# Optimization experiments

Hardware: AMD Instinct MI355X
Metric: run time of the kernel (lower is better)

The kernel has to match this reference:

```python
import jax, jax.numpy as jnp
import numpy as np

NUM_CLASS = 3
SCORE_THRESH = 0.1
NMS_THRESH = 0.25
PRE = 512    # NMS_PRE_MAXSIZE (reduced from 4096 for memory; same algorithm)
POST = 100   # NMS_POST_MAXSIZE
EPS = 1e-8


def _cross(a, b):
    return a[..., 0] * b[..., 1] - a[..., 1] * b[..., 0]


def _corners(box):
    # box: (7,) = (x, y, z, dx, dy, dz, heading) -> BEV corners (4,2), CCW
    x, y, dx, dy, r = box[0], box[1], box[3], box[4], box[6]
    c, s = jnp.cos(r), jnp.sin(r)
    lx = jnp.array([0.5, -0.5, -0.5, 0.5]) * dx
    ly = jnp.array([0.5, 0.5, -0.5, -0.5]) * dy
    return jnp.stack([x + lx * c - ly * s, y + lx * s + ly * c], axis=-1)


def _in_box(pts, box):
    # pts (P,2): point-in-rotated-rect test in the box frame
    px, py = pts[:, 0] - box[0], pts[:, 1] - box[1]
    c, s = jnp.cos(box[6]), jnp.sin(box[6])
    u = px * c + py * s
    v = -px * s + py * c
    return (jnp.abs(u) <= box[3] * 0.5 + 1e-5) & (jnp.abs(v) <= box[4] * 0.5 + 1e-5)


def _bev_inter_area(ba, bb):
    # Exact rotated-rect intersection area (same construction as the CUDA
    # iou3d kernel: inside corners + edge intersections, angle-sorted shoelace).
    ca, cb = _corners(ba), _corners(bb)
    pa, ra = ca, jnp.roll(ca, -1, 0) - ca       # edges of a
    pb, rb = cb, jnp.roll(cb, -1, 0) - cb       # edges of b
    d = _cross(ra[:, None, :], rb[None, :, :])  # (4,4)
    dsafe = jnp.where(jnp.abs(d) > EPS, d, 1.0)
    qp = pb[None, :, :] - pa[:, None, :]
    t = _cross(qp, rb[None, :, :]) / dsafe
    u = _cross(qp, ra[:, None, :]) / dsafe
    vi = (jnp.abs(d) > EPS) & (t >= 0.0) & (t <= 1.0) & (u >= 0.0) & (u <= 1.0)
    ip = pa[:, None, :] + t[..., None] * ra[:, None, :]  # (4,4,2)
    pts = jnp.concatenate([ca, cb, ip.reshape(16, 2)], 0)          # (24,2)
    val = jnp.concatenate([_in_box(ca, bb), _in_box(cb, ba), vi.reshape(16)], 0)
    cnt = val.sum()
    ctr = (pts * val[:, None]).sum(0) / jnp.maximum(cnt, 1)
    ang = jnp.where(val, jnp.arctan2(pts[:, 1] - ctr[1], pts[:, 0] - ctr[0]), 1e9)
    o = jnp.argsort(ang)
    ps, vs = pts[o], val[o]
    ps = jnp.where(vs[:, None], ps, ps[0])  # collapse invalid onto first valid pt
    area = 0.5 * jnp.abs(_cross(ps, jnp.roll(ps, -1, 0)).sum())
    return jnp.where(cnt >= 3, area, 0.0)


def _iou3d(ba, bb):
    inter = _bev_inter_area(ba, bb)
    zt = jnp.minimum(ba[2] + ba[5] * 0.5, bb[2] + bb[5] * 0.5)
    zb = jnp.maximum(ba[2] - ba[5] * 0.5, bb[2] - bb[5] * 0.5)
    i3 = inter * jnp.maximum(zt - zb, 0.0)
    va = ba[3] * ba[4] * ba[5]
    vb = bb[3] * bb[4] * bb[5]
    return i3 / jnp.maximum(va + vb - i3, EPS)


_iou_mat = jax.vmap(jax.vmap(_iou3d, (None, 0)), (0, None))


def _nms(scores, boxes):
    # scores (K,) sorted descending; greedy suppression in score order
    valid = scores >= SCORE_THRESH
    iou = _iou_mat(boxes, boxes)  # (K,K)

    def body(sup, inp):
        row, v, i = inp
        keep = v & jnp.logical_not(sup[i])
        sup = sup | (keep & (row > NMS_THRESH))
        return sup, keep

    K = scores.shape[0]
    _, keep = jax.lax.scan(body, jnp.zeros((K,), bool), (iou, valid, jnp.arange(K)))
    return keep


def _post_one(cls_logits, boxes):
    # multi_classes_nms path: cls_preds_normalized=False -> sigmoid
    scores = jax.nn.sigmoid(cls_logits)  # (N, NUM_CLASS)
    out_b, out_s, out_l = [], [], []
    for k in range(NUM_CLASS):
        s = jnp.where(scores[:, k] >= SCORE_THRESH, scores[:, k], -1.0)
        top_s, idx = jax.lax.top_k(s, PRE)
        b = boxes[idx]
        keep = _nms(top_s, b)
        ks = jnp.where(keep, top_s, -1.0)
        os_, oi = jax.lax.top_k(ks, POST)
        ov = os_ >= SCORE_THRESH
        out_b.append(jnp.where(ov[:, None], b[oi], 0.0))
        out_s.append(jnp.where(ov, os_, 0.0))
        out_l.append((k + 1) * ov.astype(jnp.int32))  # final_labels = k + 1
    return (jnp.concatenate(out_b, 0), jnp.concatenate(out_s, 0),
            jnp.concatenate(out_l, 0))


def setup_inputs() -> dict:
    key = jax.random.key(0)
    k1, k2 = jax.random.split(key)
    B, N = 2, 100000
    batch_cls_preds = jax.random.normal(k1, (B, N, NUM_CLASS), dtype=jnp.float32)
    u = jax.random.uniform(k2, (B, N, 7), dtype=jnp.float32)
    x = u[..., 0] * 70.0
    y = u[..., 1] * 80.0 - 40.0
    z = u[..., 2] * 2.0 - 1.0
    dx = u[..., 3] * 3.0 + 1.5
    dy = u[..., 4] * 1.5 + 1.2
    dz = u[..., 5] * 1.0 + 1.3
    r = u[..., 6] * 2.0 * np.pi - np.pi
    batch_box_preds = jnp.stack([x, y, z, dx, dy, dz, r], axis=-1)
    return {"batch_cls_preds": batch_cls_preds, "batch_box_preds": batch_box_preds}


def reference(batch_cls_preds, batch_box_preds):
    # returns per-batch padded (pred_boxes (B, 3*POST, 7), pred_scores, pred_labels);
    # invalid slots are zeroed (label 0 == no detection)
    return jax.vmap(_post_one)(batch_cls_preds, batch_box_preds)
```

## Files before the change

### kernel.cpp

```cpp
#include <hip/hip_runtime.h>
#include <cstdint>

#define NCLS 3
#define NPTS 100000
#define NB 2
#define PRE 512
#define POST 100
#define SCORE_TH 0.1f
#define NMS_TH 0.25
#define CAP 1024
#define NBINS 384
#define BIN_SH 17
#define BIN_OFFW (0xBD000000u >> BIN_SH)
#define FMARG 2e-5f
#define NPROB (NB * NCLS)
#define NCHUNK 98
#define CPB 4
#define NKB 25
#define WAVES_PER_PROB 2304


__device__ __forceinline__ uint32_t score_key(float x)
{
    double sd = 1.0 / (1.0 + exp(-(double)x));
    float s = (float)sd;
    if (!(s >= SCORE_TH)) s = -1.0f;
    uint32_t u = __float_as_uint(s);
    return (u & 0x80000000u) ? ~u : (u | 0x80000000u);
}

__device__ __forceinline__ float fast_sig(float x)
{
    return 1.0f / (1.0f + __expf(-x));
}

__device__ __forceinline__ int fast_bin(float s)
{
    float v = (s >= SCORE_TH) ? s : -1.0f;
    uint32_t u = __float_as_uint(v);
    uint32_t kk = (u & 0x80000000u) ? ~u : (u | 0x80000000u);
    int b = (int)(kk >> BIN_SH) - (int)BIN_OFFW;
    return b < 0 ? 0 : (b > NBINS - 1 ? NBINS - 1 : b);
}

__global__ __launch_bounds__(1024) void hist_kernel(
    const float* __restrict__ cls, uint32_t* __restrict__ hist_part,
    uint32_t* __restrict__ ctrs)
{
    __shared__ uint32_t lh[NCLS][2][NBINS];
    const int tid = threadIdx.x;
    for (int t = tid; t < NCLS * 2 * NBINS; t += 1024) ((uint32_t*)lh)[t] = 0;
    if (blockIdx.x == 0 && tid < 8) ctrs[tid] = 0;
    __syncthreads();

    const int b = blockIdx.x / NKB, kb = blockIdx.x % NKB;
    const int par = (tid >> 6) & 1;
    const float* base = cls + (size_t)b * NPTS * NCLS;
    #pragma unroll
    for (int c = 0; c < CPB; ++c) {
        int i = (kb * CPB + c) * 1024 + tid;
        if (i < NPTS) {
            const float* cp = base + (size_t)i * NCLS;
            #pragma unroll
            for (int k = 0; k < NCLS; ++k)
                atomicAdd(&lh[k][par][fast_bin(fast_sig(cp[k]))], 1u);
        }
    }
    __syncthreads();
    uint32_t* P = hist_part + (size_t)((b * NKB + kb) * NCLS) * NBINS;
    for (int t = tid; t < NCLS * NBINS; t += 1024)
        P[t] = lh[t / NBINS][0][t % NBINS] + lh[t / NBINS][1][t % NBINS];
}

__global__ __launch_bounds__(1024) void compact_kernel(
    const float* __restrict__ cls, const uint32_t* __restrict__ hist_part,
    uint32_t* __restrict__ ctrs, unsigned long long* __restrict__ cand)
{
    const int p = blockIdx.x / NCHUNK, cb = blockIdx.x % NCHUNK;
    const int b = p / NCLS, k = p % NCLS;
    const int tid = threadIdx.x;

    __shared__ unsigned long long stage[1024];
    __shared__ uint32_t sbins[NBINS];
    __shared__ uint32_t lcnt, lbase, pivot_s;

    if (tid < NBINS) sbins[tid] = 0;
    if (tid == 0) { lcnt = 0; pivot_s = 0; }
    __syncthreads();

    for (int idx = tid; idx < NKB * NBINS; idx += 1024) {
        int kb = idx / NBINS, bin = idx % NBINS;
        uint32_t v = hist_part[(size_t)((b * NKB + kb) * NCLS + k) * NBINS + bin];
        if (v) atomicAdd(&sbins[bin], v);
    }
    __syncthreads();
    for (int off = 1; off < NBINS; off <<= 1) {
        uint32_t v = 0;
        if (tid < NBINS && tid + off < NBINS) v = sbins[tid + off];
        __syncthreads();
        if (tid < NBINS) sbins[tid] += v;
        __syncthreads();
    }
    if (tid < NBINS && sbins[tid] >= PRE &&
        (tid == NBINS - 1 || sbins[tid + 1] < PRE))
        pivot_s = (uint32_t)tid;
    __syncthreads();
    const uint32_t pb = pivot_s;

    const int i = cb * 1024 + tid;
    bool sv = false;
    unsigned long long entry = 0;
    if (i < NPTS) {
        float x = cls[((size_t)b * NPTS + i) * NCLS + k];
        float sfv = fast_sig(x);
        if ((uint32_t)fast_bin(sfv + FMARG) >= pb) {
            uint32_t kk = score_key(x);
            entry = ((unsigned long long)kk << 32) | (uint32_t)(~(uint32_t)i);
            sv = true;
        }
    }
    if (sv) { uint32_t s = atomicAdd(&lcnt, 1u); stage[s] = entry; }
    __syncthreads();
    if (tid == 0 && lcnt) lbase = atomicAdd(&ctrs[p], lcnt);
    __syncthreads();
    const uint32_t n = lcnt;
    if (n) {
        const uint32_t bs = lbase;
        for (uint32_t e = tid; e < n; e += 1024) {
            uint32_t g = bs + e;
            if (g < CAP) cand[(size_t)p * CAP + g] = stage[e];
        }
    }
}

__global__ __launch_bounds__(1024) void sort_geom_kernel(
    const float* __restrict__ boxes, const unsigned long long* __restrict__ cand,
    const uint32_t* __restrict__ ctrs, uint32_t* __restrict__ cand_idx,
    float* __restrict__ cand_score, double* __restrict__ boxdata,
    float* __restrict__ screen)
{
    const int p = blockIdx.x, b = p / NCLS;
    const int tid = threadIdx.x;
    __shared__ unsigned long long skey[CAP];

    const int cnt0 = (int)ctrs[p];
    const int cnt = cnt0 < CAP ? cnt0 : CAP;
    unsigned long long val = (tid < cnt) ? cand[(size_t)p * CAP + tid] : 0ull;
    __syncthreads();

    for (int k2 = 2; k2 <= CAP; k2 <<= 1) {
        const bool up = (tid & k2) == 0;
        for (int j = k2 >> 1; j >= 64; j >>= 1) {
            skey[tid] = val;
            __syncthreads();
            unsigned long long o = skey[tid ^ j];
            __syncthreads();
            const bool keepLarge = (((tid & j) == 0) == up);
            val = keepLarge ? (val >= o ? val : o) : (val <= o ? val : o);
        }
        int js = (k2 >> 1) < 32 ? (k2 >> 1) : 32;
        for (int j = js; j >= 1; j >>= 1) {
            unsigned long long o = __shfl_xor(val, j);
            const bool keepLarge = (((tid & j) == 0) == up);
            val = keepLarge ? (val >= o ? val : o) : (val <= o ? val : o);
        }
    }

    if (tid >= PRE) return;
    unsigned long long key = val;
    double* D = boxdata + (size_t)(p * PRE + tid) * 20;
    float* S = screen + (size_t)(p * PRE + tid) * 8;
    if (key == 0ull) {
        cand_idx[p * PRE + tid] = 0;
        cand_score[p * PRE + tid] = -1.0f;
        #pragma unroll
        for (int m = 0; m < 20; ++m) D[m] = 0.0;
        #pragma unroll
        for (int m = 0; m < 8; ++m) S[m] = 0.0f;
        return;
    }
    uint32_t idx = ~((uint32_t)key);
    uint32_t ov = (uint32_t)(key >> 32);
    uint32_t ub = (ov & 0x80000000u) ? (ov ^ 0x80000000u) : ~ov;
    float sc = __uint_as_float(ub);
    cand_idx[p * PRE + tid] = idx;
    cand_score[p * PRE + tid] = sc;

    const float* bp = boxes + ((size_t)b * NPTS + idx) * 7;
    double x = bp[0], y = bp[1], z = bp[2];
    double dx = bp[3], dy = bp[4], dz = bp[5], r = bp[6];
    double c = cos(r), s = sin(r);
    double hx = 0.5 * dx, hy = 0.5 * dy;
    double zlo = z - 0.5 * dz, zhi = z + 0.5 * dz;
    double rad = sqrt(hx * hx + hy * hy);
    D[0] = x; D[1] = y; D[2] = c; D[3] = s; D[4] = hx; D[5] = hy;
    D[6] = zlo; D[7] = zhi; D[8] = dx * dy * dz; D[9] = rad;
    const double lxs[4] = { hx, -hx, -hx,  hx };
    const double lys[4] = { hy,  hy, -hy, -hy };
    #pragma unroll
    for (int m = 0; m < 4; ++m) {
        D[10 + m] = x + lxs[m] * c - lys[m] * s;
        D[14 + m] = y + lxs[m] * s + lys[m] * c;
    }
    S[0] = (float)x; S[1] = (float)y; S[2] = (float)zlo; S[3] = (float)zhi;
    S[4] = (float)rad; S[5] = 0.0f; S[6] = 0.0f; S[7] = 0.0f;
}

__global__ __launch_bounds__(256) void iou_kernel(
    const float* __restrict__ screen, const double* __restrict__ boxdata,
    unsigned long long* __restrict__ mask)
{
    const int W = blockIdx.x * 4 + (threadIdx.x >> 6);
    const int lane = threadIdx.x & 63;
    const int prob = W / WAVES_PER_PROB;
    int t = W - prob * WAVES_PER_PROB;
    int cell = t >> 6, r = t & 63;
    int wi = 0;
    while (cell >= 8 - wi) { cell -= 8 - wi; ++wi; }
    const int wj = wi + cell;
    const int bi = wi * 64 + r;
    const int j = wj * 64 + lane;

    bool surv = false;
    {
        const float* SA = screen + (size_t)(prob * PRE + bi) * 8;
        const float* SB = screen + (size_t)(prob * PRE + j) * 8;
        if (j > bi) {
            float4 a4 = *(const float4*)SA;
            float4 b4 = *(const float4*)SB;
            float hz = fminf(a4.w, b4.w) - fmaxf(a4.z, b4.z);
            if (hz > 0.0f) {
                float ddx = a4.x - b4.x, ddy = a4.y - b4.y;
                float rs = SA[4] + SB[4] + 0.01f;
                surv = (ddx * ddx + ddy * ddy <= rs * rs);
            }
        }
    }
    unsigned long long sm = __ballot(surv);
    unsigned long long supw = 0ull;
    const double* A = boxdata + (size_t)(prob * PRE + bi) * 20;

    while (sm) {
        int jb = __ffsll(sm) - 1;
        sm &= sm - 1ull;
        const int bj = wj * 64 + jb;
        const double* B = boxdata + (size_t)(prob * PRE + bj) * 20;

        double hzd = fmin(A[7], B[7]) - fmax(A[6], B[6]);
        if (hzd <= 0.0) continue;
        {
            double ddx = B[0] - A[0], ddy = B[1] - A[1];
            double ca = A[2], sa = A[3], cb2 = B[2], sb2 = B[3];
            double cd = fabs(ca * cb2 + sa * sb2);
            double sd = fabs(sa * cb2 - ca * sb2);
            double pax = fabs(ddx * ca + ddy * sa);
            double pay = fabs(-ddx * sa + ddy * ca);
            double pbx = fabs(ddx * cb2 + ddy * sb2);
            double pby = fabs(-ddx * sb2 + ddy * cb2);
            if (pax > A[4] + B[4] * cd + B[5] * sd) continue;
            if (pay > A[5] + B[4] * sd + B[5] * cd) continue;
            if (pbx > B[4] + A[4] * cd + A[5] * sd) continue;
            if (pby > B[5] + A[4] * sd + A[5] * cd) continue;
            double areaA = 4.0 * A[4] * A[5], areaB = 4.0 * B[4] * B[5];
            double i3m = fmin(areaA, areaB) * hzd;
            double den = A[8] + B[8] - i3m;
            if (den < 1e-8) den = 1e-8;
            if (!(i3m / den > (double)NMS_TH)) continue;
        }

        double PX = 0.0, PY = 0.0;
        bool valid = false;
        if (lane < 8) {
            const double* S = (lane < 4) ? A : B;
            const double* O = (lane < 4) ? B : A;
            int m = lane & 3;
            PX = S[10 + m]; PY = S[14 + m];
            double rx = PX - O[0], ry = PY - O[1];
            double u =  rx * O[2] + ry * O[3];
            double v = -rx * O[3] + ry * O[2];
            valid = (fabs(u) <= O[4] + 1e-5) && (fabs(v) <= O[5] + 1e-5);
        } else if (lane < 24) {
            int e = lane - 8, m = e >> 2, nn = e & 3;
            double ax = A[10 + m], ay = A[14 + m];
            double rax = A[10 + ((m + 1) & 3)] - ax;
            double ray = A[14 + ((m + 1) & 3)] - ay;
            double bx = B[10 + nn], by = B[14 + nn];
            double rbx = B[10 + ((nn + 1) & 3)] - bx;
            double rby = B[14 + ((nn + 1) & 3)] - by;
            double d = rax * rby - ray * rbx;
            if (fabs(d) > 1e-8) {
                double qx = bx - ax, qy = by - ay;
                double tt = (qx * rby - qy * rbx) / d;
                double uu = (qx * ray - qy * rax) / d;
                valid = (tt >= 0.0 && tt <= 1.0 && uu >= 0.0 && uu <= 1.0);
                PX = ax + tt * rax; PY = ay + tt * ray;
            }
        }
        if (!valid) { PX = 0.0; PY = 0.0; }

        unsigned long long bal = __ballot(valid);
        int cnt = __popcll(bal);
        double sx = PX, sy = PY;
        #pragma unroll
        for (int off = 16; off; off >>= 1) {
            sx += __shfl_xor(sx, off);
            sy += __shfl_xor(sy, off);
        }
        int cdiv = cnt > 0 ? cnt : 1;
        double cxc = sx / cdiv, cyc = sy / cdiv;

        double ang = valid ? atan2(PY - cyc, PX - cxc) : 1e9;
        int sidx = lane;

        #pragma unroll
        for (int k = 2; k <= 32; k <<= 1) {
            #pragma unroll
            for (int jj = k >> 1; jj > 0; jj >>= 1) {
                double oang = __shfl_xor(ang, jj);
                double opx  = __shfl_xor(PX, jj);
                double opy  = __shfl_xor(PY, jj);
                int    oidx = __shfl_xor(sidx, jj);
                bool iLow = (lane & jj) == 0;
                bool dirUp = (lane & k) == 0;
                bool mineFirst = (ang < oang) || (ang == oang && sidx < oidx);
                bool keepMine = (mineFirst == (iLow == dirUp));
                if (!keepMine) { ang = oang; PX = opx; PY = opy; sidx = oidx; }
            }
        }

        double nxp = __shfl(PX, (lane + 1) & 31);
        double nyp = __shfl(PY, (lane + 1) & 31);
        double fx  = __shfl(PX, 0);
        double fy  = __shfl(PY, 0);
        bool last = (lane == cnt - 1);
        double qx = last ? fx : nxp, qy = last ? fy : nyp;
        double contrib = 0.0;
        if (lane < cnt)
            contrib = (PX - cxc) * (qy - cyc) - (PY - cyc) * (qx - cxc);
        #pragma unroll
        for (int off = 16; off; off >>= 1) contrib += __shfl_xor(contrib, off);
        double inter = (cnt >= 3) ? 0.5 * fabs(contrib) : 0.0;

        if (lane == 0) {
            double zt = fmin(A[7], B[7]);
            double zb = fmax(A[6], B[6]);
            double hz = zt - zb;
            bool sup = false;
            if (hz > 0.0) {
                double i3 = inter * hz;
                double den = A[8] + B[8] - i3;
                if (den < 1e-8) den = 1e-8;
                sup = (i3 / den) > (double)NMS_TH;
            }
            if (sup) supw |= 1ull << jb;
        }
    }

    if (lane == 0)
        mask[(size_t)(prob * PRE + bi) * 8 + wj] = supw;
}

__global__ __launch_bounds__(256) void nms_out_kernel(
    const float* __restrict__ boxes, const uint32_t* __restrict__ cand_idx,
    const float* __restrict__ cand_score,
    const unsigned long long* __restrict__ mask, float* __restrict__ out)
{
    const int p = blockIdx.x;
    const int b = p / NCLS, k = p % NCLS;
    const int tid = threadIdx.x;

    __shared__ unsigned long long smask[PRE * 8];
    __shared__ float sscore[PRE];
    __shared__ int slist[POST];
    __shared__ int scnt;

    for (int w = tid; w < PRE * 8; w += 256)
        smask[w] = mask[(size_t)p * PRE * 8 + w];
    for (int i = tid; i < PRE; i += 256)
        sscore[i] = cand_score[p * PRE + i];
    __syncthreads();

    if (tid < 64) {
        const int ln = tid;
        unsigned long long rem = 0ull;
        #pragma unroll
        for (int w = 0; w < 8; ++w) {
            unsigned long long bw = __ballot(sscore[w * 64 + ln] >= SCORE_TH);
            if (ln == w) rem = bw;
        }
        int c = 0;
        for (;;) {
            int cv = rem ? ((ln << 6) + (__ffsll(rem) - 1)) : 4096;
            int o1 = __shfl_xor(cv, 1); cv = cv < o1 ? cv : o1;
            int o2 = __shfl_xor(cv, 2); cv = cv < o2 ? cv : o2;
            int o4 = __shfl_xor(cv, 4); cv = cv < o4 ? cv : o4;
            int i = __shfl(cv, 0);
            if (i >= 4096) break;
            if (ln == 0) slist[c] = i;
            ++c;
            if (c >= POST) break;
            unsigned long long mm = (ln < 8) ? smask[i * 8 + ln] : 0ull;
            if (ln == (i >> 6)) mm |= 1ull << (i & 63);
            rem &= ~mm;
        }
        if (ln == 0) scnt = c;
    }
    __syncthreads();

    const int cnt2 = scnt;
    for (int t2 = tid; t2 < POST; t2 += 256) {
        int row = b * (NCLS * POST) + k * POST + t2;
        float* ob = out + (size_t)row * 7;
        float* os = out + (size_t)NB * NCLS * POST * 7 + row;
        float* ol = out + (size_t)NB * NCLS * POST * 7 + (size_t)NB * NCLS * POST + row;
        if (t2 < cnt2) {
            int rr = slist[t2];
            uint32_t idx = cand_idx[p * PRE + rr];
            const float* bp = boxes + ((size_t)b * NPTS + idx) * 7;
            #pragma unroll
            for (int c7 = 0; c7 < 7; ++c7) ob[c7] = bp[c7];
            *os = sscore[rr];
            *ol = (float)(k + 1);
        } else {
            #pragma unroll
            for (int c7 = 0; c7 < 7; ++c7) ob[c7] = 0.0f;
            *os = 0.0f;
            *ol = 0.0f;
        }
    }
}

extern "C" void kernel_launch(void* const* d_in, const int* in_sizes, int n_in,
                              void* d_out, int out_size, void* d_ws, size_t ws_size,
                              hipStream_t stream)
{
    (void)in_sizes; (void)n_in; (void)out_size; (void)ws_size;
    const float* cls   = (const float*)d_in[0];
    const float* boxes = (const float*)d_in[1];
    float* out = (float*)d_out;

    char* ws = (char*)d_ws;
    uint32_t* hist_part   = (uint32_t*)(ws);
    uint32_t* ctrs        = (uint32_t*)(ws + 230400);
    unsigned long long* cand = (unsigned long long*)(ws + 230528);
    unsigned long long* mask = (unsigned long long*)(ws + 279680);
    uint32_t* cand_idx    = (uint32_t*)(ws + 476288);
    float*    cand_score  = (float*)   (ws + 488576);
    double*   boxdata     = (double*)  (ws + 500864);
    float*    screen      = (float*)   (ws + 992384);

    hipLaunchKernelGGL(hist_kernel, dim3(NB * NKB), dim3(1024), 0, stream,
                       cls, hist_part, ctrs);
    hipLaunchKernelGGL(compact_kernel, dim3(NPROB * NCHUNK), dim3(1024),
                       0, stream, cls, hist_part, ctrs, cand);
    hipLaunchKernelGGL(sort_geom_kernel, dim3(NPROB), dim3(1024), 0, stream,
                       boxes, cand, ctrs, cand_idx, cand_score, boxdata, screen);
    hipLaunchKernelGGL(iou_kernel, dim3(NPROB * WAVES_PER_PROB / 4),
                       dim3(256), 0, stream, screen, boxdata, mask);
    hipLaunchKernelGGL(nms_out_kernel, dim3(NPROB), dim3(256), 0, stream,
                       boxes, cand_idx, cand_score, mask, out);
}
```

Before: 142.6 us.

## Fuse five-kernel NMS pipeline into one persistent block per class-batch problem

Replaces the histogram, compaction, sort, IoU and NMS kernels with a single kernel that runs one 1024-thread block per (batch, class) problem. The IoU mask, screen data and candidates now stay in shared memory, and the histogram bins raw logits instead of sigmoids, which is valid because sigmoid is monotonic. This removes launch overhead and global round-trips between stages. In exchange only 6 blocks run, so each block scans 100k scores twice serially and does all the pairwise IoU work on its own, leaving most of the GPU idle.

New measurement: 408.2 us. 2.86x slower.

```diff
diff --git a/kernel.cpp b/kernel.cpp
--- a/kernel.cpp
+++ b/kernel.cpp
@@ -10,13 +10,11 @@
 #define NMS_TH 0.25
 #define CAP 1024
 #define NBINS 384
-#define BIN_SH 17
-#define BIN_OFFW (0xBD000000u >> BIN_SH)
-#define FMARG 2e-5f
+#define XBIN_SH 16
+#define XBIN_OFF (0xBFC00000u >> XBIN_SH)
+#define XMARG 2e-3f
 #define NPROB (NB * NCLS)
 #define NCHUNK 98
-#define CPB 4
-#define NKB 25
 #define WAVES_PER_PROB 2304
 
 
@@ -29,71 +27,50 @@
     return (u & 0x80000000u) ? ~u : (u | 0x80000000u);
 }
 
-__device__ __forceinline__ float fast_sig(float x)
+__device__ __forceinline__ int xbin(float x)
 {
-    return 1.0f / (1.0f + __expf(-x));
-}
-
-__device__ __forceinline__ int fast_bin(float s)
-{
-    float v = (s >= SCORE_TH) ? s : -1.0f;
-    uint32_t u = __float_as_uint(v);
-    uint32_t kk = (u & 0x80000000u) ? ~u : (u | 0x80000000u);
-    int b = (int)(kk >> BIN_SH) - (int)BIN_OFFW;
+    uint32_t u = __float_as_uint(x);
+    uint32_t key = (u & 0x80000000u) ? ~u : (u | 0x80000000u);
+    int b = (int)(key >> XBIN_SH) - (int)XBIN_OFF;
     return b < 0 ? 0 : (b > NBINS - 1 ? NBINS - 1 : b);
 }
 
-__global__ __launch_bounds__(1024) void hist_kernel(
-    const float* __restrict__ cls, uint32_t* __restrict__ hist_part,
-    uint32_t* __restrict__ ctrs)
+__global__ __launch_bounds__(1024) void mega_kernel(
+    const float* __restrict__ cls, const float* __restrict__ boxes,
+    double* __restrict__ boxdata, float* __restrict__ out)
 {
-    __shared__ uint32_t lh[NCLS][2][NBINS];
-    const int tid = threadIdx.x;
-    for (int t = tid; t < NCLS * 2 * NBINS; t += 1024) ((uint32_t*)lh)[t] = 0;
-    if (blockIdx.x == 0 && tid < 8) ctrs[tid] = 0;
-    __syncthreads();
-
-    const int b = blockIdx.x / NKB, kb = blockIdx.x % NKB;
-    const int par = (tid >> 6) & 1;
-    const float* base = cls + (size_t)b * NPTS * NCLS;
-    #pragma unroll
-    for (int c = 0; c < CPB; ++c) {
-        int i = (kb * CPB + c) * 1024 + tid;
-        if (i < NPTS) {
-            const float* cp = base + (size_t)i * NCLS;
-            #pragma unroll
-            for (int k = 0; k < NCLS; ++k)
-                atomicAdd(&lh[k][par][fast_bin(fast_sig(cp[k]))], 1u);
-        }
-    }
-    __syncthreads();
-    uint32_t* P = hist_part + (size_t)((b * NKB + kb) * NCLS) * NBINS;
-    for (int t = tid; t < NCLS * NBINS; t += 1024)
-        P[t] = lh[t / NBINS][0][t % NBINS] + lh[t / NBINS][1][t % NBINS];
-}
-
-__global__ __launch_bounds__(1024) void compact_kernel(
-    const float* __restrict__ cls, const uint32_t* __restrict__ hist_part,
-    uint32_t* __restrict__ ctrs, unsigned long long* __restrict__ cand)
-{
-    const int p = blockIdx.x / NCHUNK, cb = blockIdx.x % NCHUNK;
+    const int p = blockIdx.x;
     const int b = p / NCLS, k = p % NCLS;
     const int tid = threadIdx.x;
-
-    __shared__ unsigned long long stage[1024];
+    const int lane = tid & 63;
+    const int wv = tid >> 6;
+
+    __shared__ unsigned long long skey[CAP];
+    __shared__ unsigned long long smask[PRE * 8];
     __shared__ uint32_t sbins[NBINS];
-    __shared__ uint32_t lcnt, lbase, pivot_s;
-
-    if (tid < NBINS) sbins[tid] = 0;
+    __shared__ float sx_l[PRE], sy_l[PRE];
+    __shared__ float szlo[PRE], szhi[PRE], srad[PRE];
+    __shared__ float sscore[PRE];
+    __shared__ uint32_t sidx[PRE];
+    __shared__ int slist[POST];
+    __shared__ int scnt;
+    __shared__ uint32_t lcnt, pivot_s;
+
+    const float* cp = cls + ((size_t)b * NPTS) * NCLS + k;
+    double* Dbase = boxdata + (size_t)p * PRE * 20;
+
+    for (int t = tid; t < NBINS; t += 1024) sbins[t] = 0;
     if (tid == 0) { lcnt = 0; pivot_s = 0; }
     __syncthreads();
-
-    for (int idx = tid; idx < NKB * NBINS; idx += 1024) {
-        int kb = idx / NBINS, bin = idx % NBINS;
-        uint32_t v = hist_part[(size_t)((b * NKB + kb) * NCLS + k) * NBINS + bin];
-        if (v) atomicAdd(&sbins[bin], v);
-    }
-    __syncthreads();
+    for (int ch = 0; ch < NCHUNK; ++ch) {
+        int i = ch * 1024 + tid;
+        if (i < NPTS) {
+            int bn = xbin(cp[(size_t)i * NCLS]);
+            if (bn > 0) atomicAdd(&sbins[bn], 1u);
+        }
+    }
+    __syncthreads();
+
     for (int off = 1; off < NBINS; off <<= 1) {
         uint32_t v = 0;
         if (tid < NBINS && tid + off < NBINS) v = sbins[tid + off];
@@ -105,48 +82,26 @@
         (tid == NBINS - 1 || sbins[tid + 1] < PRE))
         pivot_s = (uint32_t)tid;
     __syncthreads();
-    const uint32_t pb = pivot_s;
-
-    const int i = cb * 1024 + tid;
-    bool sv = false;
-    unsigned long long entry = 0;
-    if (i < NPTS) {
-        float x = cls[((size_t)b * NPTS + i) * NCLS + k];
-        float sfv = fast_sig(x);
-        if ((uint32_t)fast_bin(sfv + FMARG) >= pb) {
-            uint32_t kk = score_key(x);
-            entry = ((unsigned long long)kk << 32) | (uint32_t)(~(uint32_t)i);
-            sv = true;
-        }
-    }
-    if (sv) { uint32_t s = atomicAdd(&lcnt, 1u); stage[s] = entry; }
-    __syncthreads();
-    if (tid == 0 && lcnt) lbase = atomicAdd(&ctrs[p], lcnt);
-    __syncthreads();
-    const uint32_t n = lcnt;
-    if (n) {
-        const uint32_t bs = lbase;
-        for (uint32_t e = tid; e < n; e += 1024) {
-            uint32_t g = bs + e;
-            if (g < CAP) cand[(size_t)p * CAP + g] = stage[e];
-        }
-    }
-}
-
-__global__ __launch_bounds__(1024) void sort_geom_kernel(
-    const float* __restrict__ boxes, const unsigned long long* __restrict__ cand,
-    const uint32_t* __restrict__ ctrs, uint32_t* __restrict__ cand_idx,
-    float* __restrict__ cand_score, double* __restrict__ boxdata,
-    float* __restrict__ screen)
-{
-    const int p = blockIdx.x, b = p / NCLS;
-    const int tid = threadIdx.x;
-    __shared__ unsigned long long skey[CAP];
-
-    const int cnt0 = (int)ctrs[p];
-    const int cnt = cnt0 < CAP ? cnt0 : CAP;
-    unsigned long long val = (tid < cnt) ? cand[(size_t)p * CAP + tid] : 0ull;
-    __syncthreads();
+    const int pb = (int)pivot_s;
+
+    for (int ch = 0; ch < NCHUNK; ++ch) {
+        int i = ch * 1024 + tid;
+        if (i < NPTS) {
+            float x = cp[(size_t)i * NCLS];
+            if (xbin(x + XMARG) >= pb) {
+                uint32_t kk = score_key(x);
+                uint32_t slot = atomicAdd(&lcnt, 1u);
+                if (slot < CAP)
+                    skey[slot] = ((unsigned long long)kk << 32)
+                               | (uint32_t)(~(uint32_t)i);
+            }
+        }
+    }
+    __syncthreads();
+    const uint32_t cnt = lcnt < CAP ? lcnt : CAP;
+    if (tid >= (int)cnt) skey[tid] = 0ull;
+    __syncthreads();
+    unsigned long long val = skey[tid];
 
     for (int k2 = 2; k2 <= CAP; k2 <<= 1) {
         const bool up = (tid & k2) == 0;
@@ -166,218 +121,188 @@
         }
     }
 
-    if (tid >= PRE) return;
-    unsigned long long key = val;
-    double* D = boxdata + (size_t)(p * PRE + tid) * 20;
-    float* S = screen + (size_t)(p * PRE + tid) * 8;
-    if (key == 0ull) {
-        cand_idx[p * PRE + tid] = 0;
-        cand_score[p * PRE + tid] = -1.0f;
-        #pragma unroll
-        for (int m = 0; m < 20; ++m) D[m] = 0.0;
-        #pragma unroll
-        for (int m = 0; m < 8; ++m) S[m] = 0.0f;
-        return;
-    }
-    uint32_t idx = ~((uint32_t)key);
-    uint32_t ov = (uint32_t)(key >> 32);
-    uint32_t ub = (ov & 0x80000000u) ? (ov ^ 0x80000000u) : ~ov;
-    float sc = __uint_as_float(ub);
-    cand_idx[p * PRE + tid] = idx;
-    cand_score[p * PRE + tid] = sc;
-
-    const float* bp = boxes + ((size_t)b * NPTS + idx) * 7;
-    double x = bp[0], y = bp[1], z = bp[2];
-    double dx = bp[3], dy = bp[4], dz = bp[5], r = bp[6];
-    double c = cos(r), s = sin(r);
-    double hx = 0.5 * dx, hy = 0.5 * dy;
-    double zlo = z - 0.5 * dz, zhi = z + 0.5 * dz;
-    double rad = sqrt(hx * hx + hy * hy);
-    D[0] = x; D[1] = y; D[2] = c; D[3] = s; D[4] = hx; D[5] = hy;
-    D[6] = zlo; D[7] = zhi; D[8] = dx * dy * dz; D[9] = rad;
-    const double lxs[4] = { hx, -hx, -hx,  hx };
-    const double lys[4] = { hy,  hy, -hy, -hy };
-    #pragma unroll
-    for (int m = 0; m < 4; ++m) {
-        D[10 + m] = x + lxs[m] * c - lys[m] * s;
-        D[14 + m] = y + lxs[m] * s + lys[m] * c;
-    }
-    S[0] = (float)x; S[1] = (float)y; S[2] = (float)zlo; S[3] = (float)zhi;
-    S[4] = (float)rad; S[5] = 0.0f; S[6] = 0.0f; S[7] = 0.0f;
-}
-
-__global__ __launch_bounds__(256) void iou_kernel(
-    const float* __restrict__ screen, const double* __restrict__ boxdata,
-    unsigned long long* __restrict__ mask)
-{
-    const int W = blockIdx.x * 4 + (threadIdx.x >> 6);
-    const int lane = threadIdx.x & 63;
-    const int prob = W / WAVES_PER_PROB;
-    int t = W - prob * WAVES_PER_PROB;
-    int cell = t >> 6, r = t & 63;
-    int wi = 0;
-    while (cell >= 8 - wi) { cell -= 8 - wi; ++wi; }
-    const int wj = wi + cell;
-    const int bi = wi * 64 + r;
-    const int j = wj * 64 + lane;
-
-    bool surv = false;
-    {
-        const float* SA = screen + (size_t)(prob * PRE + bi) * 8;
-        const float* SB = screen + (size_t)(prob * PRE + j) * 8;
-        if (j > bi) {
-            float4 a4 = *(const float4*)SA;
-            float4 b4 = *(const float4*)SB;
-            float hz = fminf(a4.w, b4.w) - fmaxf(a4.z, b4.z);
-            if (hz > 0.0f) {
-                float ddx = a4.x - b4.x, ddy = a4.y - b4.y;
-                float rs = SA[4] + SB[4] + 0.01f;
-                surv = (ddx * ddx + ddy * ddy <= rs * rs);
-            }
-        }
-    }
-    unsigned long long sm = __ballot(surv);
-    unsigned long long supw = 0ull;
-    const double* A = boxdata + (size_t)(prob * PRE + bi) * 20;
-
-    while (sm) {
-        int jb = __ffsll(sm) - 1;
-        sm &= sm - 1ull;
-        const int bj = wj * 64 + jb;
-        const double* B = boxdata + (size_t)(prob * PRE + bj) * 20;
-
-        double hzd = fmin(A[7], B[7]) - fmax(A[6], B[6]);
-        if (hzd <= 0.0) continue;
+    if (tid < PRE) {
+        unsigned long long key = val;
+        double* D = Dbase + (size_t)tid * 20;
+        if (key == 0ull) {
+            sidx[tid] = 0; sscore[tid] = -1.0f;
+            #pragma unroll
+            for (int m = 0; m < 20; ++m) D[m] = 0.0;
+            sx_l[tid] = 0.0f; sy_l[tid] = 0.0f;
+            szlo[tid] = 0.0f; szhi[tid] = 0.0f; srad[tid] = 0.0f;
+        } else {
+            uint32_t idx = ~((uint32_t)key);
+            uint32_t ov = (uint32_t)(key >> 32);
+            uint32_t ub = (ov & 0x80000000u) ? (ov ^ 0x80000000u) : ~ov;
+            sidx[tid] = idx;
+            sscore[tid] = __uint_as_float(ub);
+
+            const float* bp = boxes + ((size_t)b * NPTS + idx) * 7;
+            double x = bp[0], y = bp[1], z = bp[2];
+            double dx = bp[3], dy = bp[4], dz = bp[5], r = bp[6];
+            double c = cos(r), s = sin(r);
+            double hx = 0.5 * dx, hy = 0.5 * dy;
+            double zlo = z - 0.5 * dz, zhi = z + 0.5 * dz;
+            double rad = sqrt(hx * hx + hy * hy);
+            D[0] = x; D[1] = y; D[2] = c; D[3] = s; D[4] = hx; D[5] = hy;
+            D[6] = zlo; D[7] = zhi; D[8] = dx * dy * dz; D[9] = rad;
+            const double lxs[4] = { hx, -hx, -hx,  hx };
+            const double lys[4] = { hy,  hy, -hy, -hy };
+            #pragma unroll
+            for (int m = 0; m < 4; ++m) {
+                D[10 + m] = x + lxs[m] * c - lys[m] * s;
+                D[14 + m] = y + lxs[m] * s + lys[m] * c;
+            }
+            sx_l[tid] = (float)x; sy_l[tid] = (float)y;
+            szlo[tid] = (float)zlo; szhi[tid] = (float)zhi;
+            srad[tid] = (float)rad;
+        }
+    }
+    __syncthreads();
+
+    for (int t = wv; t < WAVES_PER_PROB; t += 16) {
+        int cell = t >> 6, r = t & 63;
+        int wi = 0;
+        while (cell >= 8 - wi) { cell -= 8 - wi; ++wi; }
+        const int wj = wi + cell;
+        const int bi = wi * 64 + r;
+        const int j = wj * 64 + lane;
+
+        bool surv = false;
         {
-            double ddx = B[0] - A[0], ddy = B[1] - A[1];
-            double ca = A[2], sa = A[3], cb2 = B[2], sb2 = B[3];
-            double cd = fabs(ca * cb2 + sa * sb2);
-            double sd = fabs(sa * cb2 - ca * sb2);
-            double pax = fabs(ddx * ca + ddy * sa);
-            double pay = fabs(-ddx * sa + ddy * ca);
-            double pbx = fabs(ddx * cb2 + ddy * sb2);
-            double pby = fabs(-ddx * sb2 + ddy * cb2);
-            if (pax > A[4] + B[4] * cd + B[5] * sd) continue;
-            if (pay > A[5] + B[4] * sd + B[5] * cd) continue;
-            if (pbx > B[4] + A[4] * cd + A[5] * sd) continue;
-            if (pby > B[5] + A[4] * sd + A[5] * cd) continue;
-            double areaA = 4.0 * A[4] * A[5], areaB = 4.0 * B[4] * B[5];
-            double i3m = fmin(areaA, areaB) * hzd;
-            double den = A[8] + B[8] - i3m;
-            if (den < 1e-8) den = 1e-8;
-            if (!(i3m / den > (double)NMS_TH)) continue;
-        }
-
-        double PX = 0.0, PY = 0.0;
-        bool valid = false;
-        if (lane < 8) {
-            const double* S = (lane < 4) ? A : B;
-            const double* O = (lane < 4) ? B : A;
-            int m = lane & 3;
-            PX = S[10 + m]; PY = S[14 + m];
-            double rx = PX - O[0], ry = PY - O[1];
-            double u =  rx * O[2] + ry * O[3];
-            double v = -rx * O[3] + ry * O[2];
-            valid = (fabs(u) <= O[4] + 1e-5) && (fabs(v) <= O[5] + 1e-5);
-        } else if (lane < 24) {
-            int e = lane - 8, m = e >> 2, nn = e & 3;
-            double ax = A[10 + m], ay = A[14 + m];
-            double rax = A[10 + ((m + 1) & 3)] - ax;
-            double ray = A[14 + ((m + 1) & 3)] - ay;
-            double bx = B[10 + nn], by = B[14 + nn];
-            double rbx = B[10 + ((nn + 1) & 3)] - bx;
-            double rby = B[14 + ((nn + 1) & 3)] - by;
-            double d = rax * rby - ray * rbx;
-            if (fabs(d) > 1e-8) {
-                double qx = bx - ax, qy = by - ay;
-                double tt = (qx * rby - qy * rbx) / d;
-                double uu = (qx * ray - qy * rax) / d;
-                valid = (tt >= 0.0 && tt <= 1.0 && uu >= 0.0 && uu <= 1.0);
-                PX = ax + tt * rax; PY = ay + tt * ray;
-            }
-        }
-        if (!valid) { PX = 0.0; PY = 0.0; }
-
-        unsigned long long bal = __ballot(valid);
-        int cnt = __popcll(bal);
-        double sx = PX, sy = PY;
-        #pragma unroll
-        for (int off = 16; off; off >>= 1) {
-            sx += __shfl_xor(sx, off);
-            sy += __shfl_xor(sy, off);
-        }
-        int cdiv = cnt > 0 ? cnt : 1;
-        double cxc = sx / cdiv, cyc = sy / cdiv;
-
-        double ang = valid ? atan2(PY - cyc, PX - cxc) : 1e9;
-        int sidx = lane;
-
-        #pragma unroll
-        for (int k = 2; k <= 32; k <<= 1) {
-            #pragma unroll
-            for (int jj = k >> 1; jj > 0; jj >>= 1) {
-                double oang = __shfl_xor(ang, jj);
-                double opx  = __shfl_xor(PX, jj);
-                double opy  = __shfl_xor(PY, jj);
-                int    oidx = __shfl_xor(sidx, jj);
-                bool iLow = (lane & jj) == 0;
-                bool dirUp = (lane & k) == 0;
-                bool mineFirst = (ang < oang) || (ang == oang && sidx < oidx);
-                bool keepMine = (mineFirst == (iLow == dirUp));
-                if (!keepMine) { ang = oang; PX = opx; PY = opy; sidx = oidx; }
-            }
-        }
-
-        double nxp = __shfl(PX, (lane + 1) & 31);
-        double nyp = __shfl(PY, (lane + 1) & 31);
-        double fx  = __shfl(PX, 0);
-        double fy  = __shfl(PY, 0);
-        bool last = (lane == cnt - 1);
-        double qx = last ? fx : nxp, qy = last ? fy : nyp;
-        double contrib = 0.0;
-        if (lane < cnt)
-            contrib = (PX - cxc) * (qy - cyc) - (PY - cyc) * (qx - cxc);
-        #pragma unroll
-        for (int off = 16; off; off >>= 1) contrib += __shfl_xor(contrib, off);
-        double inter = (cnt >= 3) ? 0.5 * fabs(contrib) : 0.0;
-
-        if (lane == 0) {
-            double zt = fmin(A[7], B[7]);
-            double zb = fmax(A[6], B[6]);
-            double hz = zt - zb;
-            bool sup = false;
-            if (hz > 0.0) {
-                double i3 = inter * hz;
-                double den = A[8] + B[8] - i3;
+            float ax = sx_l[bi], ay = sy_l[bi];
+            float az0 = szlo[bi], az1 = szhi[bi], ar = srad[bi];
+            if (j > bi) {
+                float hz = fminf(az1, szhi[j]) - fmaxf(az0, szlo[j]);
+                if (hz > 0.0f) {
+                    float ddx = ax - sx_l[j], ddy = ay - sy_l[j];
+                    float rs = ar + srad[j] + 0.01f;
+                    surv = (ddx * ddx + ddy * ddy <= rs * rs);
+                }
+            }
+        }
+        unsigned long long sm = __ballot(surv);
+        unsigned long long supw = 0ull;
+        const double* A = Dbase + (size_t)bi * 20;
+
+        while (sm) {
+            int jb = __ffsll(sm) - 1;
+            sm &= sm - 1ull;
+            const double* B = Dbase + (size_t)(wj * 64 + jb) * 20;
+
+            double hzd = fmin(A[7], B[7]) - fmax(A[6], B[6]);
+            if (hzd <= 0.0) continue;
+            {
+                double ddx = B[0] - A[0], ddy = B[1] - A[1];
+                double ca = A[2], sa = A[3], cb2 = B[2], sb2 = B[3];
+                double cd = fabs(ca * cb2 + sa * sb2);
+                double sd = fabs(sa * cb2 - ca * sb2);
+                double pax = fabs(ddx * ca + ddy * sa);
+                double pay = fabs(-ddx * sa + ddy * ca);
+                double pbx = fabs(ddx * cb2 + ddy * sb2);
+                double pby = fabs(-ddx * sb2 + ddy * cb2);
+                if (pax > A[4] + B[4] * cd + B[5] * sd) continue;
+                if (pay > A[5] + B[4] * sd + B[5] * cd) continue;
+                if (pbx > B[4] + A[4] * cd + A[5] * sd) continue;
+                if (pby > B[5] + A[4] * sd + A[5] * cd) continue;
+                double areaA = 4.0 * A[4] * A[5], areaB = 4.0 * B[4] * B[5];
+                double i3m = fmin(areaA, areaB) * hzd;
+                double den = A[8] + B[8] - i3m;
                 if (den < 1e-8) den = 1e-8;
-                sup = (i3 / den) > (double)NMS_TH;
-            }
-            if (sup) supw |= 1ull << jb;
-        }
-    }
-
-    if (lane == 0)
-        mask[(size_t)(prob * PRE + bi) * 8 + wj] = supw;
-}
-
-__global__ __launch_bounds__(256) void nms_out_kernel(
-    const float* __restrict__ boxes, const uint32_t* __restrict__ cand_idx,
-    const float* __restrict__ cand_score,
-    const unsigned long long* __restrict__ mask, float* __restrict__ out)
-{
-    const int p = blockIdx.x;
-    const int b = p / NCLS, k = p % NCLS;
-    const int tid = threadIdx.x;
-
-    __shared__ unsigned long long smask[PRE * 8];
-    __shared__ float sscore[PRE];
-    __shared__ int slist[POST];
-    __shared__ int scnt;
-
-    for (int w = tid; w < PRE * 8; w += 256)
-        smask[w] = mask[(size_t)p * PRE * 8 + w];
-    for (int i = tid; i < PRE; i += 256)
-        sscore[i] = cand_score[p * PRE + i];
+                if (!(i3m / den > (double)NMS_TH)) continue;
+            }
+
+            double PX = 0.0, PY = 0.0;
+            bool valid = false;
+            if (lane < 8) {
+                const double* S = (lane < 4) ? A : B;
+                const double* O = (lane < 4) ? B : A;
+                int m = lane & 3;
+                PX = S[10 + m]; PY = S[14 + m];
+                double rx = PX - O[0], ry = PY - O[1];
+                double u =  rx * O[2] + ry * O[3];
+                double v = -rx * O[3] + ry * O[2];
+                valid = (fabs(u) <= O[4] + 1e-5) && (fabs(v) <= O[5] + 1e-5);
+            } else if (lane < 24) {
+                int e = lane - 8, m = e >> 2, nn = e & 3;
+                double ax = A[10 + m], ay = A[14 + m];
+                double rax = A[10 + ((m + 1) & 3)] - ax;
+                double ray = A[14 + ((m + 1) & 3)] - ay;
+                double bx = B[10 + nn], by = B[14 + nn];
+                double rbx = B[10 + ((nn + 1) & 3)] - bx;
+                double rby = B[14 + ((nn + 1) & 3)] - by;
+                double d = rax * rby - ray * rbx;
+                if (fabs(d) > 1e-8) {
+                    double qx = bx - ax, qy = by - ay;
+                    double tt = (qx * rby - qy * rbx) / d;
+                    double uu = (qx * ray - qy * rax) / d;
+                    valid = (tt >= 0.0 && tt <= 1.0 && uu >= 0.0 && uu <= 1.0);
+                    PX = ax + tt * rax; PY = ay + tt * ray;
+                }
+            }
+            if (!valid) { PX = 0.0; PY = 0.0; }
+
+            unsigned long long bal = __ballot(valid);
+            int cntv = __popcll(bal);
+            double sx = PX, sy = PY;
+            #pragma unroll
+            for (int off = 16; off; off >>= 1) {
+                sx += __shfl_xor(sx, off);
+                sy += __shfl_xor(sy, off);
+            }
+            int cdiv = cntv > 0 ? cntv : 1;
+            double cxc = sx / cdiv, cyc = sy / cdiv;
+
+            double ang = valid ? atan2(PY - cyc, PX - cxc) : 1e9;
+            int sidx2 = lane;
+
+            #pragma unroll
+            for (int kk2 = 2; kk2 <= 32; kk2 <<= 1) {
+                #pragma unroll
+                for (int jj = kk2 >> 1; jj > 0; jj >>= 1) {
+                    double oang = __shfl_xor(ang, jj);
+                    double opx  = __shfl_xor(PX, jj);
+                    double opy  = __shfl_xor(PY, jj);
+                    int    oidx = __shfl_xor(sidx2, jj);
+                    bool iLow = (lane & jj) == 0;
+                    bool dirUp = (lane & kk2) == 0;
+                    bool mineFirst = (ang < oang) || (ang == oang && sidx2 < oidx);
+                    bool keepMine = (mineFirst == (iLow == dirUp));
+                    if (!keepMine) { ang = oang; PX = opx; PY = opy; sidx2 = oidx; }
+                }
+            }
+
+            double nxp = __shfl(PX, (lane + 1) & 31);
+            double nyp = __shfl(PY, (lane + 1) & 31);
+            double fx  = __shfl(PX, 0);
+            double fy  = __shfl(PY, 0);
+            bool last = (lane == cntv - 1);
+            double qx = last ? fx : nxp, qy = last ? fy : nyp;
+            double contrib = 0.0;
+            if (lane < cntv)
+                contrib = (PX - cxc) * (qy - cyc) - (PY - cyc) * (qx - cxc);
+            #pragma unroll
+            for (int off = 16; off; off >>= 1) contrib += __shfl_xor(contrib, off);
+            double inter = (cntv >= 3) ? 0.5 * fabs(contrib) : 0.0;
+
+            if (lane == 0) {
+                double zt = fmin(A[7], B[7]);
+                double zb = fmax(A[6], B[6]);
+                double hz = zt - zb;
+                bool sup = false;
+                if (hz > 0.0) {
+                    double i3 = inter * hz;
+                    double den = A[8] + B[8] - i3;
+                    if (den < 1e-8) den = 1e-8;
+                    sup = (i3 / den) > (double)NMS_TH;
+                }
+                if (sup) supw |= 1ull << jb;
+            }
+        }
+
+        if (lane == 0)
+            smask[bi * 8 + wj] = supw;
+    }
     __syncthreads();
 
     if (tid < 64) {
@@ -408,14 +333,15 @@
     __syncthreads();
 
     const int cnt2 = scnt;
-    for (int t2 = tid; t2 < POST; t2 += 256) {
+    for (int t2 = tid; t2 < POST; t2 += 1024) {
         int row = b * (NCLS * POST) + k * POST + t2;
         float* ob = out + (size_t)row * 7;
         float* os = out + (size_t)NB * NCLS * POST * 7 + row;
-        float* ol = out + (size_t)NB * NCLS * POST * 7 + (size_t)NB * NCLS * POST + row;
+        float* ol = out + (size_t)NB * NCLS * POST * 7
+                        + (size_t)NB * NCLS * POST + row;
         if (t2 < cnt2) {
             int rr = slist[t2];
-            uint32_t idx = cand_idx[p * PRE + rr];
+            uint32_t idx = sidx[rr];
             const float* bp = boxes + ((size_t)b * NPTS + idx) * 7;
             #pragma unroll
             for (int c7 = 0; c7 < 7; ++c7) ob[c7] = bp[c7];
@@ -438,25 +364,8 @@
     const float* cls   = (const float*)d_in[0];
     const float* boxes = (const float*)d_in[1];
     float* out = (float*)d_out;
-
-    char* ws = (char*)d_ws;
-    uint32_t* hist_part   = (uint32_t*)(ws);
-    uint32_t* ctrs        = (uint32_t*)(ws + 230400);
-    unsigned long long* cand = (unsigned long long*)(ws + 230528);
-    unsigned long long* mask = (unsigned long long*)(ws + 279680);
-    uint32_t* cand_idx    = (uint32_t*)(ws + 476288);
-    float*    cand_score  = (float*)   (ws + 488576);
-    double*   boxdata     = (double*)  (ws + 500864);
-    float*    screen      = (float*)   (ws + 992384);
-
-    hipLaunchKernelGGL(hist_kernel, dim3(NB * NKB), dim3(1024), 0, stream,
-                       cls, hist_part, ctrs);
-    hipLaunchKernelGGL(compact_kernel, dim3(NPROB * NCHUNK), dim3(1024),
-                       0, stream, cls, hist_part, ctrs, cand);
-    hipLaunchKernelGGL(sort_geom_kernel, dim3(NPROB), dim3(1024), 0, stream,
-                       boxes, cand, ctrs, cand_idx, cand_score, boxdata, screen);
-    hipLaunchKernelGGL(iou_kernel, dim3(NPROB * WAVES_PER_PROB / 4),
-                       dim3(256), 0, stream, screen, boxdata, mask);
-    hipLaunchKernelGGL(nms_out_kernel, dim3(NPROB), dim3(256), 0, stream,
-                       boxes, cand_idx, cand_score, mask, out);
+    double* boxdata = (double*)d_ws;
+
+    hipLaunchKernelGGL(mega_kernel, dim3(NPROB), dim3(1024), 0, stream,
+                       cls, boxes, boxdata, out);
 }
```
